# Kernel tuning notes

Measured on AMD Instinct MI355X. Metric: run time of the kernel, lower is better.

Reference implementation:

```python
import jax, jax.numpy as jnp
import numpy as np

N = 30000       # nodes
E = 480000      # edges (before self-loops)
G = 64          # graphs in batch
IN = 128        # in_channels
HID = 128       # hidden_dim
HEADS = 4
NEG_SLOPE = 0.2


def gat_layer(x, src, dst, W, att_src, att_dst, b):
    """PyG-style GATConv: W [Fin, H*C], att_* [H, C], b [H*C]. Returns [N, H*C] (head concat)."""
    H, C = att_src.shape
    h = (x @ W).reshape(-1, H, C)                      # [N, H, C]
    a_s = jnp.einsum('nhc,hc->nh', h, att_src)         # [N, H]
    a_d = jnp.einsum('nhc,hc->nh', h, att_dst)
    e = jax.nn.leaky_relu(a_s[src] + a_d[dst], NEG_SLOPE)   # [Etot, H]
    # segment softmax over edges grouped by destination node
    m = jax.ops.segment_max(e, dst, num_segments=N)
    e = jnp.exp(e - m[dst])
    denom = jax.ops.segment_sum(e, dst, num_segments=N)
    alpha = e / (denom[dst] + 1e-16)                   # [Etot, H]
    msg = h[src] * alpha[:, :, None]                   # [Etot, H, C]
    out = jax.ops.segment_sum(msg, dst, num_segments=N)
    return out.reshape(-1, H * C) + b


def setup_inputs():
    key = jax.random.key(0)
    ks = jax.random.split(key, 13)
    s = 0.05
    x = jax.random.normal(ks[0], (N, IN), jnp.float32)
    edge_index = jax.random.randint(ks[1], (2, E), 0, N, dtype=jnp.int32)
    batch = jnp.sort(jax.random.randint(ks[2], (N,), 0, G, dtype=jnp.int32))
    return {
        'x': x,
        'edge_index': edge_index,
        'batch': batch,
        'W1': jax.random.normal(ks[3], (IN, HEADS * HID), jnp.float32) * s,
        'att_src1': jax.random.normal(ks[4], (HEADS, HID), jnp.float32) * s,
        'att_dst1': jax.random.normal(ks[5], (HEADS, HID), jnp.float32) * s,
        'b1': jnp.zeros((HEADS * HID,), jnp.float32),
        'W2': jax.random.normal(ks[6], (HEADS * HID, HID), jnp.float32) * s,
        'att_src2': jax.random.normal(ks[7], (1, HID), jnp.float32) * s,
        'att_dst2': jax.random.normal(ks[8], (1, HID), jnp.float32) * s,
        'b2': jnp.zeros((HID,), jnp.float32),
        'lin_w': jax.random.normal(ks[9], (HID, 1), jnp.float32) * s,
        'lin_b': jnp.zeros((1,), jnp.float32),
    }


def reference(x, edge_index, batch, W1, att_src1, att_dst1, b1, W2, att_src2, att_dst2, b2, lin_w, lin_b):
    # add self-loops (PyG GATConv default)
    loop = jnp.arange(N, dtype=edge_index.dtype)
    src = jnp.concatenate([edge_index[0], loop])
    dst = jnp.concatenate([edge_index[1], loop])

    h = gat_layer(x, src, dst, W1, att_src1, att_dst1, b1)   # [N, 4*HID]
    h = jax.nn.elu(h)
    h = gat_layer(h, src, dst, W2, att_src2, att_dst2, b2)   # [N, HID]
    h = jax.nn.elu(h)

    # global mean pool over graphs
    sums = jax.ops.segment_sum(h, batch, num_segments=G)     # [G, HID]
    cnts = jax.ops.segment_sum(jnp.ones((N,), h.dtype), batch, num_segments=G)
    pooled = sums / jnp.maximum(cnts, 1.0)[:, None]

    out = pooled @ lin_w + lin_b                             # [G, 1]
    return out.squeeze(-1)                                   # [G]
```

## Files before the change

kernel.cpp:

```cpp
#include <hip/hip_runtime.h>

#define NN    30000
#define EE    480000
#define ETOT  (EE + NN)
#define GG    64
#define IN_CH 128
#define HID   128
#define HEADS 4
#define F1    (HEADS * HID)
#define CAP   64

typedef __attribute__((ext_vector_type(8))) __bf16 bf16x8;
typedef __attribute__((ext_vector_type(4))) float  floatx4;
typedef __attribute__((ext_vector_type(2))) float  f32x2;

__device__ __forceinline__ float lrelu(float x) { return x > 0.f ? x : 0.2f * x; }
__device__ __forceinline__ float elu_f(float x) { return x > 0.f ? x : (expf(x) - 1.f); }
__device__ __forceinline__ unsigned short f2bf(float f) {
    unsigned int u = __float_as_uint(f);
    return (unsigned short)((u + 0x7FFFu + ((u >> 16) & 1u)) >> 16);
}
__device__ __forceinline__ float bf2f(unsigned short u) {
    return __uint_as_float(((unsigned int)u) << 16);
}
__device__ __forceinline__ f32x2 fma2(float a, f32x2 v, f32x2 acc) {
    f32x2 av = {a, a};
    return __builtin_elementwise_fma(av, v, acc);
}

#define LDW 136
__global__ __launch_bounds__(256) void gemm12_k(const unsigned short* __restrict__ agg,
                                                const unsigned short* __restrict__ W1t,
                                                const unsigned short* __restrict__ W2t,
                                                const float* __restrict__ b1,
                                                unsigned short* __restrict__ hh2,
                                                const float* __restrict__ ws,
                                                const float* __restrict__ wd,
                                                float* __restrict__ as_out,
                                                float* __restrict__ ad_out,
                                                int M)
{
    __shared__ unsigned short Bl[128 * LDW];
    __shared__ unsigned short H1c[128 * LDW];

    const int tid  = threadIdx.x;
    const int w    = tid >> 6, lane = tid & 63;
    const int quad = lane >> 4, l16 = lane & 15;
    const int bm   = blockIdx.x * 128;

    floatx4 zf = {0.f, 0.f, 0.f, 0.f};
    floatx4 acc2[2][8];
#pragma unroll
    for (int rt = 0; rt < 2; rt++)
#pragma unroll
        for (int ct = 0; ct < 8; ct++) acc2[rt][ct] = zf;

    for (int h = 0; h < 4; h++) {
        uint4 av[2][4];
#pragma unroll
        for (int rt = 0; rt < 2; rt++) {
            int r = bm + w * 32 + rt * 16 + l16;
#pragma unroll
            for (int kb = 0; kb < 4; kb++)
                av[rt][kb] = (r < M)
                    ? *(const uint4*)(agg + (size_t)r * F1 + h * 128 + kb * 32 + quad * 8)
                    : uint4{0, 0, 0, 0};
        }
        float bb[8];
#pragma unroll
        for (int ct = 0; ct < 8; ct++) bb[ct] = b1[h * 128 + ct * 16 + l16];

        if (h) __syncthreads();
#pragma unroll
        for (int i = 0; i < 8; i++) {
            int j = i * 256 + tid;
            int n = j >> 4, ko = (j & 15) * 8;
            *(uint4*)&Bl[n * LDW + ko] = *(const uint4*)(W1t + h * 16384 + n * 128 + ko);
        }
        __syncthreads();

        floatx4 acc1[2][8];
#pragma unroll
        for (int rt = 0; rt < 2; rt++)
#pragma unroll
            for (int ct = 0; ct < 8; ct++) acc1[rt][ct] = zf;
#pragma unroll
        for (int kb = 0; kb < 4; kb++) {
            bf16x8 bfr[8];
#pragma unroll
            for (int ct = 0; ct < 8; ct++)
                bfr[ct] = *(bf16x8*)&Bl[(ct * 16 + l16) * LDW + kb * 32 + quad * 8];
#pragma unroll
            for (int rt = 0; rt < 2; rt++) {
                bf16x8 a = *(bf16x8*)&av[rt][kb];
#pragma unroll
                for (int ct = 0; ct < 8; ct++)
                    acc1[rt][ct] = __builtin_amdgcn_mfma_f32_16x16x32_bf16(a, bfr[ct], acc1[rt][ct], 0, 0, 0);
            }
        }

#pragma unroll
        for (int rt = 0; rt < 2; rt++)
#pragma unroll
            for (int ct = 0; ct < 8; ct++)
#pragma unroll
                for (int reg = 0; reg < 4; reg++) {
                    float v = elu_f(acc1[rt][ct][reg] + bb[ct]);
                    H1c[(w * 32 + rt * 16 + quad * 4 + reg) * LDW + ct * 16 + l16] = f2bf(v);
                }
        __syncthreads();
#pragma unroll
        for (int i = 0; i < 8; i++) {
            int j = i * 256 + tid;
            int n = j >> 4, ko = (j & 15) * 8;
            *(uint4*)&Bl[n * LDW + ko] = *(const uint4*)(W2t + (size_t)n * F1 + h * 128 + ko);
        }
        __syncthreads();

#pragma unroll
        for (int kb = 0; kb < 4; kb++) {
            bf16x8 af[2], bfr[8];
#pragma unroll
            for (int rt = 0; rt < 2; rt++)
                af[rt] = *(bf16x8*)&H1c[(w * 32 + rt * 16 + l16) * LDW + kb * 32 + quad * 8];
#pragma unroll
            for (int ct = 0; ct < 8; ct++)
                bfr[ct] = *(bf16x8*)&Bl[(ct * 16 + l16) * LDW + kb * 32 + quad * 8];
#pragma unroll
            for (int rt = 0; rt < 2; rt++)
#pragma unroll
                for (int ct = 0; ct < 8; ct++)
                    acc2[rt][ct] = __builtin_amdgcn_mfma_f32_16x16x32_bf16(af[rt], bfr[ct], acc2[rt][ct], 0, 0, 0);
        }
    }

    __syncthreads();
#pragma unroll
    for (int rt = 0; rt < 2; rt++)
#pragma unroll
        for (int ct = 0; ct < 8; ct++)
#pragma unroll
            for (int reg = 0; reg < 4; reg++)
                Bl[(w * 32 + rt * 16 + quad * 4 + reg) * 128 + ct * 16 + l16] =
                    f2bf(acc2[rt][ct][reg]);
    __syncthreads();
#pragma unroll
    for (int i = 0; i < 8; i++) {
        int j = i * 256 + tid;
        int rl = j >> 4, off = (j & 15) * 8;
        int row = bm + rl;
        if (row < M)
            *(uint4*)(hh2 + (size_t)row * HID + off) = *(uint4*)&Bl[rl * 128 + off];
    }
#pragma unroll
    for (int rt = 0; rt < 2; rt++) {
        int rl = w * 32 + rt * 16 + l16;
        int row = bm + rl;
        const unsigned short* rowp = &Bl[rl * 128 + quad * 32];
        float ps = 0.f, pd = 0.f;
#pragma unroll
        for (int jj = 0; jj < 32; jj++) {
            float hv = bf2f(rowp[jj]);
            ps = fmaf(hv, ws[quad * 32 + jj], ps);
            pd = fmaf(hv, wd[quad * 32 + jj], pd);
        }
        ps += __shfl_xor(ps, 16); ps += __shfl_xor(ps, 32);
        pd += __shfl_xor(pd, 16); pd += __shfl_xor(pd, 32);
        if (quad == 0 && row < M) { as_out[row] = ps; ad_out[row] = pd; }
    }
}

__global__ void prep_k(const float* __restrict__ W1, const float* __restrict__ W2,
                       const float* __restrict__ att_s, const float* __restrict__ att_d,
                       unsigned short* __restrict__ W1t, unsigned short* __restrict__ W2t,
                       float* __restrict__ wt, int* __restrict__ deg,
                       float* __restrict__ pooled_cnt)
{
    int b = blockIdx.x;
    if (b < 256) {
        int idx = b * 256 + threadIdx.x;
        int h = idx >> 14, rem = idx & 16383, n = rem >> 7, k = rem & 127;
        W1t[idx] = f2bf(W1[(size_t)k * F1 + h * 128 + n]);
    } else if (b < 512) {
        int idx = (b - 256) * 256 + threadIdx.x;
        int n = idx >> 9, k = idx & 511;
        W2t[idx] = f2bf(W2[(size_t)k * HID + n]);
    } else if (b < 520) {
        if (threadIdx.x < 128) {
            int q = b - 512;
            int h = q & 3, sd = q >> 2;
            int i = threadIdx.x;
            const float* att = (sd ? att_d : att_s) + h * 128;
            const float* wr = W1 + (size_t)i * F1 + h * 128;
            float acc = 0.f;
            for (int c = 0; c < 128; c++) acc = fmaf(wr[c], att[c], acc);
            wt[sd * 512 + h * 128 + i] = acc;
        }
    } else if (b < 638) {
        int i = (b - 520) * 256 + threadIdx.x;
        if (i < NN) deg[i] = 0;
    } else {
        int i = (b - 638) * 256 + threadIdx.x;
        if (i < GG * HID + GG) pooled_cnt[i] = 0.f;
    }
}

#define SCORE_BLKS ((NN + 31) / 32)
__global__ __launch_bounds__(256) void scorefill_k(const float* __restrict__ x,
                                                   const float* __restrict__ wt,
                                                   float* __restrict__ a_s,
                                                   float* __restrict__ a_d,
                                                   unsigned short* __restrict__ x16,
                                                   const int* __restrict__ ei,
                                                   int* __restrict__ deg,
                                                   int* __restrict__ perm)
{
    int b = blockIdx.x;
    int t = threadIdx.x;
    if (b < SCORE_BLKS) {
        __shared__ __align__(16) float swt[1024];
        ((float4*)swt)[t] = ((const float4*)wt)[t];
        __syncthreads();
        const int node0 = b * 32;
        int node = node0 + (t >> 3);
        int q = t & 7;
        int h = q & 3, sd = q >> 2;
        if (node < NN) {
            const float4* xr = (const float4*)(x + (size_t)node * IN_CH);
            const float4* wr = (const float4*)(swt + sd * 512 + h * 128);
            float acc = 0.f;
#pragma unroll 4
            for (int c = 0; c < 32; c++) {
                float4 xv = xr[c], wv = wr[c];
                acc = fmaf(xv.x, wv.x, acc);
                acc = fmaf(xv.y, wv.y, acc);
                acc = fmaf(xv.z, wv.z, acc);
                acc = fmaf(xv.w, wv.w, acc);
            }
            if (sd == 0) a_s[node * 4 + h] = acc;
            else         a_d[node * 4 + h] = acc;
        }
        int col = t & 127;
#pragma unroll 4
        for (int r = (t >> 7); r < 32; r += 2) {
            int nr = node0 + r;
            if (nr < NN)
                x16[(size_t)nr * IN_CH + col] = f2bf(x[(size_t)nr * IN_CH + col]);
        }
    } else {
        int i = (b - SCORE_BLKS) * 256 + t;
        if (i < ETOT) {
            int s, d;
            if (i < EE) { s = ei[i]; d = ei[EE + i]; }
            else        { s = i - EE; d = i - EE; }
            int p = atomicAdd(&deg[d], 1);
            if (p < CAP) perm[(size_t)d * CAP + p] = s;
        }
    }
}

__global__ __launch_bounds__(256) void gat_agg1w(const unsigned short* __restrict__ x16,
                                                 const float* __restrict__ a_s,
                                                 const float* __restrict__ a_d,
                                                 const int* __restrict__ deg,
                                                 const int* __restrict__ perm,
                                                 unsigned short* __restrict__ agg)
{
    __shared__ int    sSrc[4][64];
    __shared__ __align__(16) float4 sE[4][64];
    const int wave = threadIdx.x >> 6;
    const int lane = threadIdx.x & 63;
    const int hw   = lane >> 5;
    const int c4   = (lane & 31) * 4;
    int n = blockIdx.x * 4 + wave;
    if (n >= NN) return;
    const int rem = min(deg[n], CAP);
    const float4 ad4 = *(const float4*)(a_d + (size_t)n * 4);

    if (lane < rem) {
        int sj = perm[(size_t)n * CAP + lane];
        float4 av = *(const float4*)(a_s + (size_t)sj * 4);
        sSrc[wave][lane] = sj;
        sE[wave][lane] = make_float4(__expf(lrelu(av.x + ad4.x)), __expf(lrelu(av.y + ad4.y)),
                                     __expf(lrelu(av.z + ad4.z)), __expf(lrelu(av.w + ad4.w)));
    }
    __builtin_amdgcn_wave_barrier();

    f32x2 aLo[4] = {{0,0},{0,0},{0,0},{0,0}};
    f32x2 aHi[4] = {{0,0},{0,0},{0,0},{0,0}};
    f32x2 den01 = {0,0}, den23 = {0,0};

    for (int j = hw; j < rem; j += 2) {
        int s = sSrc[wave][j];
        float4 ev = sE[wave][j];
        den01 += (f32x2){ev.x, ev.y};
        den23 += (f32x2){ev.z, ev.w};
        uint2 uv = *(const uint2*)(x16 + (size_t)s * IN_CH + c4);
        f32x2 xlo = { __uint_as_float(uv.x << 16), __uint_as_float(uv.x & 0xFFFF0000u) };
        f32x2 xhi = { __uint_as_float(uv.y << 16), __uint_as_float(uv.y & 0xFFFF0000u) };
        aLo[0] = fma2(ev.x, xlo, aLo[0]); aHi[0] = fma2(ev.x, xhi, aHi[0]);
        aLo[1] = fma2(ev.y, xlo, aLo[1]); aHi[1] = fma2(ev.y, xhi, aHi[1]);
        aLo[2] = fma2(ev.z, xlo, aLo[2]); aHi[2] = fma2(ev.z, xhi, aHi[2]);
        aLo[3] = fma2(ev.w, xlo, aLo[3]); aHi[3] = fma2(ev.w, xhi, aHi[3]);
    }
#pragma unroll
    for (int h = 0; h < 4; h++) {
        aLo[h].x += __shfl_xor(aLo[h].x, 32); aLo[h].y += __shfl_xor(aLo[h].y, 32);
        aHi[h].x += __shfl_xor(aHi[h].x, 32); aHi[h].y += __shfl_xor(aHi[h].y, 32);
    }
    den01.x += __shfl_xor(den01.x, 32); den01.y += __shfl_xor(den01.y, 32);
    den23.x += __shfl_xor(den23.x, 32); den23.y += __shfl_xor(den23.y, 32);
    const float iv0 = 1.f / (den01.x + 1e-16f), iv1 = 1.f / (den01.y + 1e-16f);
    const float iv2 = 1.f / (den23.x + 1e-16f), iv3 = 1.f / (den23.y + 1e-16f);

#pragma unroll
    for (int k = 0; k < 2; k++) {
        int h = hw * 2 + k;
        f32x2 lo = hw ? aLo[2 + k] : aLo[k];
        f32x2 hi = hw ? aHi[2 + k] : aHi[k];
        float iv = hw ? (k ? iv3 : iv2) : (k ? iv1 : iv0);
        uint2 o;
        o.x = (unsigned)f2bf(lo.x * iv) | ((unsigned)f2bf(lo.y * iv) << 16);
        o.y = (unsigned)f2bf(hi.x * iv) | ((unsigned)f2bf(hi.y * iv) << 16);
        *(uint2*)(agg + (size_t)n * F1 + h * 128 + c4) = o;
    }
}

__global__ __launch_bounds__(256) void gat_agg2w(const unsigned short* __restrict__ h16,
                                                 const float* __restrict__ a_s,
                                                 const float* __restrict__ a_d,
                                                 const int* __restrict__ deg,
                                                 const int* __restrict__ perm,
                                                 const float* __restrict__ bias,
                                                 unsigned short* __restrict__ out16)
{
    int n = blockIdx.x * 4 + (threadIdx.x >> 6);
    if (n >= NN) return;
    const int lane = threadIdx.x & 63;
    const int hw   = lane >> 5;
    const int c4   = (lane & 31) * 4;
    const int rem = min(deg[n], CAP);
    const float ad = a_d[n];

    int sj = 0; float e = 0.f;
    if (lane < rem) {
        sj = perm[(size_t)n * CAP + lane];
        e = __expf(lrelu(a_s[sj] + ad));
    }
    f32x2 accLo = {0,0}, accHi = {0,0};
    float den = 0.f;
    for (int j = hw; j < rem; j += 2) {
        int   s = __shfl(sj, j);
        float a = __shfl(e, j);
        den += a;
        uint2 uv = *(const uint2*)(h16 + (size_t)s * HID + c4);
        f32x2 lo = { __uint_as_float(uv.x << 16), __uint_as_float(uv.x & 0xFFFF0000u) };
        f32x2 hi = { __uint_as_float(uv.y << 16), __uint_as_float(uv.y & 0xFFFF0000u) };
        accLo = fma2(a, lo, accLo);
        accHi = fma2(a, hi, accHi);
    }
    accLo.x += __shfl_xor(accLo.x, 32); accLo.y += __shfl_xor(accLo.y, 32);
    accHi.x += __shfl_xor(accHi.x, 32); accHi.y += __shfl_xor(accHi.y, 32);
    den += __shfl_xor(den, 32);
    const float inv = 1.f / (den + 1e-16f);
    if (hw == 0) {
        float4 bb = *(const float4*)(bias + c4);
        uint2 o;
        o.x = (unsigned)f2bf(elu_f(accLo.x * inv + bb.x)) |
              ((unsigned)f2bf(elu_f(accLo.y * inv + bb.y)) << 16);
        o.y = (unsigned)f2bf(elu_f(accHi.x * inv + bb.z)) |
              ((unsigned)f2bf(elu_f(accHi.y * inv + bb.w)) << 16);
        *(uint2*)(out16 + (size_t)n * HID + c4) = o;
    }
}

#define NPB 64
__global__ __launch_bounds__(128) void pool_seg_k(const unsigned short* __restrict__ out16,
                                                  const int* __restrict__ batch,
                                                  float* __restrict__ pooled,
                                                  float* __restrict__ cnt)
{
    int n0 = blockIdx.x * NPB;
    int n1 = min(n0 + NPB, NN);
    if (n0 >= n1) return;
    int t = threadIdx.x;
    int cur = batch[n0];
    float acc = 0.f;
    int count = 0;
    for (int n = n0; n < n1; n++) {
        int g = batch[n];
        if (g != cur) {
            atomicAdd(&pooled[cur * HID + t], acc);
            if (t == 0) atomicAdd(&cnt[cur], (float)count);
            acc = 0.f; count = 0; cur = g;
        }
        acc += bf2f(out16[(size_t)n * HID + t]);
        count++;
    }
    atomicAdd(&pooled[cur * HID + t], acc);
    if (t == 0) atomicAdd(&cnt[cur], (float)count);
}

__global__ void final_k(const float* __restrict__ pooled, const float* __restrict__ cnt,
                        const float* __restrict__ lw, const float* __restrict__ lb,
                        float* __restrict__ outp)
{
    int g = threadIdx.x;
    if (g < GG) {
        float acc = 0.f;
        for (int c = 0; c < HID; c++) acc += pooled[g * HID + c] * lw[c];
        float cc = fmaxf(cnt[g], 1.0f);
        outp[g] = acc / cc + lb[0];
    }
}

extern "C" void kernel_launch(void* const* d_in, const int* in_sizes, int n_in,
                              void* d_out, int out_size, void* d_ws, size_t ws_size,
                              hipStream_t stream)
{
    const float* x    = (const float*)d_in[0];
    const int*   ei   = (const int*)d_in[1];
    const int*   batch= (const int*)d_in[2];
    const float* W1   = (const float*)d_in[3];
    const float* as1w = (const float*)d_in[4];
    const float* ad1w = (const float*)d_in[5];
    const float* b1   = (const float*)d_in[6];
    const float* W2   = (const float*)d_in[7];
    const float* as2w = (const float*)d_in[8];
    const float* ad2w = (const float*)d_in[9];
    const float* b2   = (const float*)d_in[10];
    const float* lw   = (const float*)d_in[11];
    const float* lb   = (const float*)d_in[12];
    float* outp = (float*)d_out;

    char* w = (char*)d_ws;
    size_t off = 0;
    auto alloc = [&](size_t bytes) -> char* {
        char* p = w + off;
        off += (bytes + 255) & ~(size_t)255;
        return p;
    };
    char*  reg0   = alloc((size_t)NN * F1 * 2);
    char*  reg1   = alloc((size_t)NN * HID * 2 * 2);
    unsigned short* x16 = (unsigned short*)alloc((size_t)NN * IN_CH * 2);
    unsigned short* W1t = (unsigned short*)alloc(65536 * 2);
    unsigned short* W2t = (unsigned short*)alloc(65536 * 2);
    float* wt1    = (float*)alloc(1024 * 4);
    float* a_s1   = (float*)alloc((size_t)NN * 4 * 4);
    float* a_d1   = (float*)alloc((size_t)NN * 4 * 4);
    float* a_s2   = (float*)alloc((size_t)NN * 4);
    float* a_d2   = (float*)alloc((size_t)NN * 4);
    int*   deg    = (int*)alloc((size_t)NN * 4);
    int*   perm   = (int*)alloc((size_t)NN * CAP * 4);
    float* pooled = (float*)alloc((size_t)(GG * HID + GG) * 4);
    float* cnt    = pooled + GG * HID;

    unsigned short* agg16   = (unsigned short*)reg0;
    unsigned short* hh2_16  = (unsigned short*)reg1;
    unsigned short* out2_16 = (unsigned short*)reg1 + (size_t)NN * HID;

    prep_k<<<671, 256, 0, stream>>>(W1, W2, as1w, ad1w, W1t, W2t, wt1, deg, pooled);

    const int FILL_BLKS = (ETOT + 255) / 256;
    scorefill_k<<<SCORE_BLKS + FILL_BLKS, 256, 0, stream>>>(x, wt1, a_s1, a_d1, x16,
                                                            ei, deg, perm);

    gat_agg1w<<<(NN + 3) / 4, 256, 0, stream>>>(x16, a_s1, a_d1, deg, perm, agg16);

    gemm12_k<<<(NN + 127) / 128, 256, 0, stream>>>(agg16, W1t, W2t, b1, hh2_16,
                                                   as2w, ad2w, a_s2, a_d2, NN);

    gat_agg2w<<<(NN + 3) / 4, 256, 0, stream>>>(hh2_16, a_s2, a_d2, deg, perm, b2, out2_16);

    pool_seg_k<<<(NN + NPB - 1) / NPB, 128, 0, stream>>>(out2_16, batch, pooled, cnt);
    final_k<<<1, 64, 0, stream>>>(pooled, cnt, lw, lb, outp);
}
```

Baseline: 241.7 us.

## Drop shared-memory weight staging and make fused GEMM waves fully independent

The fused two-layer GEMM kernel no longer stages W1 and W2 tiles in shared memory behind block-wide barriers. Each wave now loads its B fragments straight from global memory (served by L1/L2) and uses its own private 32-row hidden buffer, so the `__syncthreads` calls become wave barriers. This removes block synchronisation stalls and roughly halves the shared-memory footprint, which may allow more blocks per CU. In exchange, every wave re-fetches the full weight slices from cache, which increases global/L2 load traffic and latency exposure in the MFMA loops.

New measurement: 270.0 us. +11.7%, slower.

```diff
diff --git a/kernel.cpp b/kernel.cpp
--- a/kernel.cpp
+++ b/kernel.cpp
@@ -40,13 +40,13 @@
                                                 float* __restrict__ ad_out,
                                                 int M)
 {
-    __shared__ unsigned short Bl[128 * LDW];
-    __shared__ unsigned short H1c[128 * LDW];
+    __shared__ unsigned short H1c[4][32 * LDW];
 
     const int tid  = threadIdx.x;
     const int w    = tid >> 6, lane = tid & 63;
     const int quad = lane >> 4, l16 = lane & 15;
-    const int bm   = blockIdx.x * 128;
+    const int bm   = blockIdx.x * 128 + w * 32;
+    unsigned short* Hw = &H1c[w][0];
 
     floatx4 zf = {0.f, 0.f, 0.f, 0.f};
     floatx4 acc2[2][8];
@@ -59,7 +59,7 @@
         uint4 av[2][4];
 #pragma unroll
         for (int rt = 0; rt < 2; rt++) {
-            int r = bm + w * 32 + rt * 16 + l16;
+            int r = bm + rt * 16 + l16;
 #pragma unroll
             for (int kb = 0; kb < 4; kb++)
                 av[rt][kb] = (r < M)
@@ -70,15 +70,6 @@
 #pragma unroll
         for (int ct = 0; ct < 8; ct++) bb[ct] = b1[h * 128 + ct * 16 + l16];
 
-        if (h) __syncthreads();
-#pragma unroll
-        for (int i = 0; i < 8; i++) {
-            int j = i * 256 + tid;
-            int n = j >> 4, ko = (j & 15) * 8;
-            *(uint4*)&Bl[n * LDW + ko] = *(const uint4*)(W1t + h * 16384 + n * 128 + ko);
-        }
-        __syncthreads();
-
         floatx4 acc1[2][8];
 #pragma unroll
         for (int rt = 0; rt < 2; rt++)
@@ -86,19 +77,19 @@
             for (int ct = 0; ct < 8; ct++) acc1[rt][ct] = zf;
 #pragma unroll
         for (int kb = 0; kb < 4; kb++) {
-            bf16x8 bfr[8];
-#pragma unroll
-            for (int ct = 0; ct < 8; ct++)
-                bfr[ct] = *(bf16x8*)&Bl[(ct * 16 + l16) * LDW + kb * 32 + quad * 8];
-#pragma unroll
-            for (int rt = 0; rt < 2; rt++) {
-                bf16x8 a = *(bf16x8*)&av[rt][kb];
-#pragma unroll
-                for (int ct = 0; ct < 8; ct++)
-                    acc1[rt][ct] = __builtin_amdgcn_mfma_f32_16x16x32_bf16(a, bfr[ct], acc1[rt][ct], 0, 0, 0);
+#pragma unroll
+            for (int ct = 0; ct < 8; ct++) {
+                bf16x8 bfr = *(const bf16x8*)(W1t + h * 16384 + (ct * 16 + l16) * 128
+                                              + kb * 32 + quad * 8);
+#pragma unroll
+                for (int rt = 0; rt < 2; rt++) {
+                    bf16x8 a = *(bf16x8*)&av[rt][kb];
+                    acc1[rt][ct] = __builtin_amdgcn_mfma_f32_16x16x32_bf16(a, bfr, acc1[rt][ct], 0, 0, 0);
+                }
             }
         }
 
+        __builtin_amdgcn_wave_barrier();
 #pragma unroll
         for (int rt = 0; rt < 2; rt++)
 #pragma unroll
@@ -106,57 +97,49 @@
 #pragma unroll
                 for (int reg = 0; reg < 4; reg++) {
                     float v = elu_f(acc1[rt][ct][reg] + bb[ct]);
-                    H1c[(w * 32 + rt * 16 + quad * 4 + reg) * LDW + ct * 16 + l16] = f2bf(v);
+                    Hw[(rt * 16 + quad * 4 + reg) * LDW + ct * 16 + l16] = f2bf(v);
                 }
-        __syncthreads();
-#pragma unroll
-        for (int i = 0; i < 8; i++) {
-            int j = i * 256 + tid;
-            int n = j >> 4, ko = (j & 15) * 8;
-            *(uint4*)&Bl[n * LDW + ko] = *(const uint4*)(W2t + (size_t)n * F1 + h * 128 + ko);
-        }
-        __syncthreads();
+        __builtin_amdgcn_wave_barrier();
 
 #pragma unroll
         for (int kb = 0; kb < 4; kb++) {
-            bf16x8 af[2], bfr[8];
+            bf16x8 af[2];
 #pragma unroll
             for (int rt = 0; rt < 2; rt++)
-                af[rt] = *(bf16x8*)&H1c[(w * 32 + rt * 16 + l16) * LDW + kb * 32 + quad * 8];
-#pragma unroll
-            for (int ct = 0; ct < 8; ct++)
-                bfr[ct] = *(bf16x8*)&Bl[(ct * 16 + l16) * LDW + kb * 32 + quad * 8];
-#pragma unroll
-            for (int rt = 0; rt < 2; rt++)
-#pragma unroll
-                for (int ct = 0; ct < 8; ct++)
-                    acc2[rt][ct] = __builtin_amdgcn_mfma_f32_16x16x32_bf16(af[rt], bfr[ct], acc2[rt][ct], 0, 0, 0);
-        }
-    }
-
-    __syncthreads();
+                af[rt] = *(bf16x8*)&Hw[(rt * 16 + l16) * LDW + kb * 32 + quad * 8];
+#pragma unroll
+            for (int ct = 0; ct < 8; ct++) {
+                bf16x8 bfr = *(const bf16x8*)(W2t + (size_t)(ct * 16 + l16) * F1 + h * 128
+                                              + kb * 32 + quad * 8);
+#pragma unroll
+                for (int rt = 0; rt < 2; rt++)
+                    acc2[rt][ct] = __builtin_amdgcn_mfma_f32_16x16x32_bf16(af[rt], bfr, acc2[rt][ct], 0, 0, 0);
+            }
+        }
+    }
+
+    __builtin_amdgcn_wave_barrier();
 #pragma unroll
     for (int rt = 0; rt < 2; rt++)
 #pragma unroll
         for (int ct = 0; ct < 8; ct++)
 #pragma unroll
             for (int reg = 0; reg < 4; reg++)
-                Bl[(w * 32 + rt * 16 + quad * 4 + reg) * 128 + ct * 16 + l16] =
-                    f2bf(acc2[rt][ct][reg]);
-    __syncthreads();
+                Hw[(rt * 16 + quad * 4 + reg) * 128 + ct * 16 + l16] = f2bf(acc2[rt][ct][reg]);
+    __builtin_amdgcn_wave_barrier();
 #pragma unroll
     for (int i = 0; i < 8; i++) {
-        int j = i * 256 + tid;
+        int j = i * 64 + lane;
         int rl = j >> 4, off = (j & 15) * 8;
         int row = bm + rl;
         if (row < M)
-            *(uint4*)(hh2 + (size_t)row * HID + off) = *(uint4*)&Bl[rl * 128 + off];
+            *(uint4*)(hh2 + (size_t)row * HID + off) = *(uint4*)&Hw[rl * 128 + off];
     }
 #pragma unroll
     for (int rt = 0; rt < 2; rt++) {
-        int rl = w * 32 + rt * 16 + l16;
+        int rl = rt * 16 + l16;
         int row = bm + rl;
-        const unsigned short* rowp = &Bl[rl * 128 + quad * 32];
+        const unsigned short* rowp = &Hw[rl * 128 + quad * 32];
         float ps = 0.f, pd = 0.f;
 #pragma unroll
         for (int jj = 0; jj < 32; jj++) {
```
